# Performance work log

Hardware: AMD Instinct MI355X
Metric: run time of the kernel (lower is better)

The kernel has to match this reference:

```python
import jax, jax.numpy as jnp
from jax import lax
import numpy as np

T, B, H, L = 512, 64, 512, 2


def _ran_layer(x, c0, w_ih, w_hh, b, length):
    """x: [T,B,H], c0: [B,H]; returns (output [T,B,H], c_T [B,H])."""
    wi = jnp.einsum('tbi,ih->tbh', x, w_ih)  # precompute input projections

    def step(c, inp):
        t, x_t, wi_t = inp
        g = c @ w_hh + b + wi_t                      # [B, 2H]
        f, i = jnp.split(g, 2, axis=1)
        c1 = jax.nn.sigmoid(i) * x_t + jax.nn.sigmoid(f) * jnp.tanh(c)
        mask = (t < length)[:, None].astype(c1.dtype)  # length-mask blend
        c1 = c1 * mask + c * (1.0 - mask)
        return c1, c1

    ts = jnp.arange(x.shape[0])
    cT, out = lax.scan(step, c0, (ts, x, wi))
    return out, cT


def setup_inputs() -> dict:
    key = jax.random.key(0)
    ks = jax.random.split(key, 8)
    stdv = 1.0 / np.sqrt(H)

    def u(k, shape):
        return jax.random.uniform(k, shape, jnp.float32, -stdv, stdv)

    return {
        'input_': jax.random.normal(ks[0], (T, B, H), jnp.float32),
        'hx': jnp.zeros((L, B, H), jnp.float32),
        'length': jax.random.randint(ks[1], (B,), 0, T, jnp.int64 if jax.config.jax_enable_x64 else jnp.int32),
        'w_ih_0': u(ks[2], (H, 2 * H)),
        'w_hh_0': u(ks[3], (H, 2 * H)),
        'b_0': jnp.zeros((2 * H,), jnp.float32),
        'w_ih_1': u(ks[4], (H, 2 * H)),
        'w_hh_1': u(ks[5], (H, 2 * H)),
        'b_1': jnp.zeros((2 * H,), jnp.float32),
    }


def reference(input_, hx, length, w_ih_0, w_hh_0, b_0, w_ih_1, w_hh_1, b_1):
    params = [(w_ih_0, w_hh_0, b_0), (w_ih_1, w_hh_1, b_1)]
    x = input_
    c_n = []
    for layer in range(L):
        w_ih, w_hh, b = params[layer]
        x, cT = _ran_layer(x, hx[layer], w_ih, w_hh, b, length)
        c_n.append(cT)
    return x, jnp.stack(c_n, 0)
```

## Files before the change

### kernel.cpp

```cpp
#include <hip/hip_runtime.h>

#define T_ 512
#define B_ 64
#define H_ 512
#define G_ 1024

typedef _Float16 f16;
typedef _Float16 h2 __attribute__((ext_vector_type(2)));
typedef _Float16 h4 __attribute__((ext_vector_type(4)));
typedef _Float16 f16x8 __attribute__((ext_vector_type(8)));
typedef float f32x4 __attribute__((ext_vector_type(4)));
typedef unsigned long long u64;

#define SPINMAX (1 << 22)

__device__ __forceinline__ float dot8_h(uint4 w, uint4 c, float acc) {
    union U { uint4 u; h2 h[4]; };
    U uw; uw.u = w;
    U uc; uc.u = c;
#if defined(__has_builtin) && __has_builtin(__builtin_amdgcn_fdot2)
    acc = __builtin_amdgcn_fdot2(uw.h[0], uc.h[0], acc, false);
    acc = __builtin_amdgcn_fdot2(uw.h[1], uc.h[1], acc, false);
    acc = __builtin_amdgcn_fdot2(uw.h[2], uc.h[2], acc, false);
    acc = __builtin_amdgcn_fdot2(uw.h[3], uc.h[3], acc, false);
#else
#pragma unroll
    for (int i = 0; i < 4; ++i) {
        acc += (float)uw.h[i][0] * (float)uc.h[i][0];
        acc += (float)uw.h[i][1] * (float)uc.h[i][1];
    }
#endif
    return acc;
}

__device__ __forceinline__ float sigm(float x) { return 1.f / (1.f + __expf(-x)); }

__device__ __forceinline__ u64 ldA64(const u64* p) {
    return __hip_atomic_load(p, __ATOMIC_RELAXED, __HIP_MEMORY_SCOPE_AGENT);
}
__device__ __forceinline__ void stA32(unsigned* p, unsigned v) {
    __hip_atomic_store(p, v, __ATOMIC_RELAXED, __HIP_MEMORY_SCOPE_AGENT);
}

__global__ void pack_fp16(const float* __restrict__ src, uint4* __restrict__ dst) {
    int idx = blockIdx.x * 256 + threadIdx.x;
    int j  = idx & (G_ - 1);
    int k8 = idx >> 10;
    union U { uint4 u; f16 h[8]; } v;
#pragma unroll
    for (int i = 0; i < 8; ++i)
        v.h[i] = (f16)src[(size_t)(k8 * 8 + i) * G_ + j];
    dst[idx] = v.u;
}

__global__ void pack_wcols(const float* __restrict__ src, uint4* __restrict__ dst) {
    int idx = blockIdx.x * 256 + threadIdx.x;
    int col = idx & 1023, k2 = idx >> 10;
    union U { uint4 u; f16 h[8]; } v;
#pragma unroll
    for (int i = 0; i < 8; ++i)
        v.h[i] = (f16)src[(size_t)(k2 * 8 + i) * G_ + col];
    dst[(size_t)col * 64 + k2] = v.u;
}

__global__ void pack_xf16(const float* __restrict__ src, f16* __restrict__ dst) {
    int idx = blockIdx.x * 256 + threadIdx.x;
    float4 a = ((const float4*)src)[idx * 2];
    float4 b = ((const float4*)src)[idx * 2 + 1];
    f16x8 v = {(f16)a.x, (f16)a.y, (f16)a.z, (f16)a.w,
               (f16)b.x, (f16)b.y, (f16)b.z, (f16)b.w};
    *(f16x8*)&dst[idx * 8] = v;
}

__global__ void pack_wT(const float* __restrict__ w, f16* __restrict__ bt) {
    int idx = blockIdx.x * 256 + threadIdx.x;
    int k = idx & 511, n = idx >> 9;
    bt[idx] = (f16)w[(size_t)k * G_ + n];
}

__launch_bounds__(256, 2)
__global__ void mfma_gemm(const f16* __restrict__ A, const f16* __restrict__ BT,
                          const float* __restrict__ bias, f16* __restrict__ C) {
    __shared__ __align__(16) f16 aLds[128][64 + 8];
    __shared__ __align__(16) f16 bLds[128][64 + 8];
    const int tid = threadIdx.x;
    const int bm = blockIdx.x, bn = blockIdx.y;
    const int lane = tid & 63, wid = tid >> 6;
    const int wm = wid & 1, wn = wid >> 1;
    const int fr = lane & 15, fg = lane >> 4;

    f32x4 acc[4][4] = {};

    for (int kt = 0; kt < 8; ++kt) {
#pragma unroll
        for (int p = 0; p < 4; ++p) {
            int i = p * 256 + tid;
            int row = i >> 3, slot = i & 7;
            uint4 av = *(const uint4*)&A[((size_t)(bm * 128 + row)) * 512 + kt * 64 + slot * 8];
            uint4 bv = *(const uint4*)&BT[((size_t)(bn * 128 + row)) * 512 + kt * 64 + slot * 8];
            *(uint4*)&aLds[row][slot * 8] = av;
            *(uint4*)&bLds[row][slot * 8] = bv;
        }
        __syncthreads();
#pragma unroll
        for (int kf = 0; kf < 2; ++kf) {
            const int k0 = kf * 32 + fg * 8;
            f16x8 af[4], bf[4];
#pragma unroll
            for (int mi = 0; mi < 4; ++mi)
                af[mi] = *(const f16x8*)&aLds[wm * 64 + mi * 16 + fr][k0];
#pragma unroll
            for (int ni = 0; ni < 4; ++ni)
                bf[ni] = *(const f16x8*)&bLds[wn * 64 + ni * 16 + fr][k0];
#pragma unroll
            for (int mi = 0; mi < 4; ++mi)
#pragma unroll
                for (int ni = 0; ni < 4; ++ni)
                    acc[mi][ni] = __builtin_amdgcn_mfma_f32_16x16x32_f16(
                        af[mi], bf[ni], acc[mi][ni], 0, 0, 0);
        }
        __syncthreads();
    }

#pragma unroll
    for (int mi = 0; mi < 4; ++mi) {
#pragma unroll
        for (int ni = 0; ni < 4; ++ni) {
            int n = bn * 128 + wn * 64 + ni * 16 + fr;
            float bv = bias[n];
#pragma unroll
            for (int r = 0; r < 4; ++r) {
                int m = bm * 128 + wm * 64 + mi * 16 + fg * 4 + r;
                C[(size_t)m * G_ + n] = (f16)(acc[mi][ni][r] + bv);
            }
        }
    }
}

#define GM 128
#define GN 64
#define GK 16
__launch_bounds__(256)
__global__ void gemm_bias_f16(const float* __restrict__ A,
                              const float* __restrict__ Bm,
                              const float* __restrict__ bias,
                              f16* __restrict__ C, int M) {
    __shared__ __align__(16) float Als[GK][GM + 4];
    __shared__ __align__(16) float Bls[GK][GN];
    int tid = threadIdx.x;
    int m_base = blockIdx.x * GM;
    int n_base = blockIdx.y * GN;
    int tx = tid & 15, ty = tid >> 4;
    int m0 = ty * 8, n0 = tx * 4;
    float acc[8][4] = {};

    for (int k0 = 0; k0 < H_; k0 += GK) {
#pragma unroll
        for (int r = 0; r < 2; ++r) {
            int idx2 = tid + 256 * r;
            int row = idx2 >> 2, kc = (idx2 & 3) * 4;
            float4 av = *(const float4*)&A[(size_t)(m_base + row) * H_ + k0 + kc];
            Als[kc + 0][row] = av.x;
            Als[kc + 1][row] = av.y;
            Als[kc + 2][row] = av.z;
            Als[kc + 3][row] = av.w;
        }
        {
            int kk = tid >> 4, colb = (tid & 15) * 4;
            float4 bv = *(const float4*)&Bm[(size_t)(k0 + kk) * G_ + n_base + colb];
            *(float4*)&Bls[kk][colb] = bv;
        }
        __syncthreads();
#pragma unroll
        for (int kk = 0; kk < GK; ++kk) {
            float a0[8], b0[4];
            *(float4*)&a0[0] = *(const float4*)&Als[kk][m0];
            *(float4*)&a0[4] = *(const float4*)&Als[kk][m0 + 4];
            *(float4*)&b0[0] = *(const float4*)&Bls[kk][n0];
#pragma unroll
            for (int im = 0; im < 8; ++im)
#pragma unroll
                for (int in = 0; in < 4; ++in)
                    acc[im][in] += a0[im] * b0[in];
        }
        __syncthreads();
    }
    float bv[4];
    *(float4*)&bv[0] = *(const float4*)&bias[n_base + n0];
#pragma unroll
    for (int im = 0; im < 8; ++im) {
        h4 hv;
#pragma unroll
        for (int in = 0; in < 4; ++in) hv[in] = (f16)(acc[im][in] + bv[in]);
        *(h4*)&C[(size_t)(m_base + m0 + im) * G_ + n_base + n0] = hv;
    }
}

template <int PATH>
__launch_bounds__(1024, 1)
__global__ void ran_scan(const float* __restrict__ x_in, float* __restrict__ x_out,
                         float* __restrict__ c_out, const float* __restrict__ c0,
                         const int* __restrict__ length,
                         const uint4* __restrict__ whh_p,
                         const f16* __restrict__ wi, const float* __restrict__ bias,
                         const float* __restrict__ whh_f, const float* __restrict__ wih_f) {
    __shared__ __align__(16) f16 c_h[H_];
    __shared__ __align__(16) float c_f32[H_];
    __shared__ __align__(16) float x_f32[H_];
    __shared__ float g_i_lds[H_];

    const int b = blockIdx.x, tid = threadIdx.x;
    int len = length[b];
    if (len < 0) len = 0;
    if (len > T_) len = T_;

    float c1 = 0.f;
    if (tid < H_) {
        c1 = c0[(size_t)b * H_ + tid];
        c_h[tid] = (f16)c1;
        if (PATH == 2) c_f32[tid] = c1;
    }
    const float bj = (PATH == 0) ? 0.f : bias[tid];
    __syncthreads();

    for (int t = 0; t < len; ++t) {
        const size_t base = ((size_t)t * B_ + b) * H_;
        float xv = 0.f;
        if (tid < H_) {
            xv = x_in[base + tid];
            if (PATH == 2) x_f32[tid] = xv;
        }
        if (PATH == 2) __syncthreads();

        float g;
        if (PATH == 0) g = (float)wi[((size_t)t * B_ + b) * G_ + tid];
        else           g = bj;

        if (PATH == 0) {
            const uint4* cc = (const uint4*)c_h;
#pragma unroll 4
            for (int k8 = 0; k8 < H_ / 8; ++k8)
                g = dot8_h(whh_p[(size_t)k8 * G_ + tid], cc[k8], g);
        } else {
#pragma unroll 2
            for (int k = 0; k < H_; k += 4) {
                float4 cv = *(const float4*)&c_f32[k];
                g += cv.x * whh_f[(size_t)(k + 0) * G_ + tid];
                g += cv.y * whh_f[(size_t)(k + 1) * G_ + tid];
                g += cv.z * whh_f[(size_t)(k + 2) * G_ + tid];
                g += cv.w * whh_f[(size_t)(k + 3) * G_ + tid];
            }
#pragma unroll 2
            for (int k = 0; k < H_; k += 4) {
                float4 xvv = *(const float4*)&x_f32[k];
                g += xvv.x * wih_f[(size_t)(k + 0) * G_ + tid];
                g += xvv.y * wih_f[(size_t)(k + 1) * G_ + tid];
                g += xvv.z * wih_f[(size_t)(k + 2) * G_ + tid];
                g += xvv.w * wih_f[(size_t)(k + 3) * G_ + tid];
            }
        }

        if (tid >= H_) g_i_lds[tid - H_] = g;
        __syncthreads();
        if (tid < H_) {
            float gi = g_i_lds[tid];
            float c_old = c1;
            c1 = sigm(gi) * xv + sigm(g) * tanhf(c_old);
            c_h[tid] = (f16)c1;
            if (PATH == 2) c_f32[tid] = c1;
            x_out[base + tid] = c1;
        }
        __syncthreads();
    }

    if (tid < H_) {
        for (int t = len; t < T_; ++t)
            x_out[((size_t)t * B_ + b) * H_ + tid] = c1;
        c_out[(size_t)b * H_ + tid] = c1;
    }
}

__global__ __launch_bounds__(512, 1)
void scan_mfma(const float* __restrict__ x_in, const f16* __restrict__ wi,
               const uint4* __restrict__ wpack, const float* __restrict__ c0,
               const int* __restrict__ length, float* __restrict__ out,
               float* __restrict__ cn, unsigned* __restrict__ cbuf,
               int base_tag) {
    __shared__ __align__(16) f16 c_h[2][H_];
    __shared__ __align__(16) float2 g_buf[128];
    __shared__ float c_fin[2][64];

    const int tid = threadIdx.x;
    const int bg = blockIdx.x & 31, s = blockIdx.x >> 5;
    const int b0 = bg * 2;
    const int w = tid >> 6, lane = tid & 63;
    const int n16 = lane & 15, kg = lane >> 4;

    const int gc = w * 16 + n16;
    const int gcol = (gc < 64) ? (s * 64 + gc) : (512 + s * 64 + (gc - 64));
    uint4 wreg[16];
    {
        const uint4* wp = wpack + (size_t)gcol * 64 + kg;
#pragma unroll
        for (int m = 0; m < 16; ++m) wreg[m] = wp[m * 4];
    }

    {
        float a = c0[(size_t)b0 * H_ + tid];
        float b = c0[(size_t)(b0 + 1) * H_ + tid];
        c_h[0][tid] = (f16)a;
        c_h[1][tid] = (f16)b;
    }
    int len0 = length[b0], len1 = length[b0 + 1];
    len0 = min(max(len0, 0), T_);
    len1 = min(max(len1, 0), T_);
    const int maxlen = max(len0, len1);

    const int ab = (n16 < 2) ? n16 : 1;
    const int fb = tid >> 6, fcol = tid & 63;
    const int jj = s * 64 + fcol;
    const int myb = b0 + fb;
    const int mylen = fb ? len1 : len0;
    float c_old = 0.f;
    if (tid < 128) c_old = c0[(size_t)myb * H_ + jj];
    __syncthreads();

    for (int t = 0; t < maxlen; ++t) {
        float xv = 0.f, wif = 0.f, wii = 0.f;
        if (tid < 128) {
            size_t rb = (size_t)t * B_ + myb;
            xv  = x_in[rb * H_ + jj];
            wif = (float)wi[rb * G_ + jj];
            wii = (float)wi[rb * G_ + 512 + jj];
        }

        {
            f32x4 acc = {};
#pragma unroll
            for (int m = 0; m < 16; ++m) {
                f16x8 af = *(const f16x8*)&c_h[ab][m * 32 + kg * 8];
                acc = __builtin_amdgcn_mfma_f32_16x16x32_f16(
                    af, *(const f16x8*)&wreg[m], acc, 0, 0, 0);
            }
            if (lane < 16)
                g_buf[w * 16 + lane] = make_float2(acc[0], acc[1]);
        }
        __syncthreads();

        const int p1 = (t + 1) & 1;
        const unsigned tagw = (unsigned)(base_tag + t + 1) & 0xffffu;

        if (tid < 128) {
            float2 vf = g_buf[fcol];
            float2 vi = g_buf[64 + fcol];
            float gf = (fb ? vf.y : vf.x) + wif;
            float gi = (fb ? vi.y : vi.x) + wii;
            float c1;
            if (t < mylen) {
                float e2 = __expf(2.f * c_old);
                float th = (e2 - 1.f) / (e2 + 1.f);
                c1 = sigm(gi) * xv + sigm(gf) * th;
            } else {
                c1 = c_old;
            }
            c_old = c1;
            union { f16 h; unsigned short u; } cv;
            cv.h = (f16)c1;
            stA32(&cbuf[((size_t)(p1 * B_ + myb) << 9) + jj],
                  (tagw << 16) | (unsigned)cv.u);
            out[((size_t)t * B_ + myb) * H_ + jj] = c1;
            c_h[fb][jj] = cv.h;
        }

        if (t + 1 < maxlen) {
            int bidx = tid >> 8;
            int e = (tid & 255) * 2;
            if ((unsigned)(e - s * 64) >= 64u) {
                const u64 want2 = ((u64)tagw << 48) | ((u64)tagw << 16);
                const u64 mask2 = 0xffff0000ffff0000ull;
                const u64* pb = (const u64*)(cbuf +
                                   ((size_t)(p1 * B_ + b0 + bidx) << 9) + e);
                u64 v = ldA64(pb);
                int gd = 0;
                while ((v & mask2) != want2) {
                    if (++gd > SPINMAX) break;
                    if (gd > 16) __builtin_amdgcn_s_sleep(2);
                    v = ldA64(pb);
                }
                unsigned lo = (unsigned)v & 0xffffu;
                unsigned hi = (unsigned)(v >> 32) & 0xffffu;
                *(unsigned*)&c_h[bidx][e] = lo | (hi << 16);
            }
        }
        __syncthreads();
    }

    if (tid < 128) {
        c_fin[fb][fcol] = c_old;
        cn[(size_t)myb * H_ + jj] = c_old;
    }
    __syncthreads();

    const int ntail = T_ - maxlen;
    for (int i = tid; i < ntail * 128; i += 512) {
        int tb = i >> 7;
        int cc = i & 127;
        int tfb = cc >> 6, tfc = cc & 63;
        out[((size_t)(maxlen + tb) * B_ + b0 + tfb) * H_ + s * 64 + tfc] =
            c_fin[tfb][tfc];
    }
}

__global__ __launch_bounds__(512, 1)
void scan_vgpr(const float* __restrict__ x_in, const f16* __restrict__ wi,
               const uint4* __restrict__ wpack, const float* __restrict__ c0,
               const int* __restrict__ length, float* __restrict__ out,
               float* __restrict__ cn, unsigned* __restrict__ cbuf,
               int base_tag) {
    __shared__ __align__(16) f16 c_h[2][H_];
    __shared__ float red[2][128][5];
    __shared__ float c_fin[2][64];

    const int tid = threadIdx.x;
    const int bg = blockIdx.x & 31, s = blockIdx.x >> 5;
    const int b0 = bg * 2;
    const int col = tid & 127, kq = tid >> 7;

    const int gcol = s * 64 + (col & 63) + ((col >> 6) << 9);
    uint4 wreg[16];
    {
        const uint4* wp = wpack + (size_t)gcol * 64 + kq * 16;
#pragma unroll
        for (int i = 0; i < 16; ++i) wreg[i] = wp[i];
    }

    {
        float a = c0[(size_t)b0 * H_ + tid];
        float b = c0[(size_t)(b0 + 1) * H_ + tid];
        c_h[0][tid] = (f16)a;
        c_h[1][tid] = (f16)b;
    }
    int len0 = length[b0], len1 = length[b0 + 1];
    len0 = min(max(len0, 0), T_);
    len1 = min(max(len1, 0), T_);
    const int maxlen = max(len0, len1);

    const int fb = tid >> 6, fcol = tid & 63;
    const int jj = s * 64 + fcol;
    const int myb = b0 + fb;
    const int mylen = fb ? len1 : len0;
    float c_old = 0.f;
    if (tid < 128) c_old = c0[(size_t)myb * H_ + jj];
    __syncthreads();

    for (int t = 0; t < maxlen; ++t) {
        float xv = 0.f, wif = 0.f, wii = 0.f;
        if (tid < 128) {
            size_t rb = (size_t)t * B_ + myb;
            xv  = x_in[rb * H_ + jj];
            wif = (float)wi[rb * G_ + jj];
            wii = (float)wi[rb * G_ + 512 + jj];
        }

        {
            const uint4* cA = (const uint4*)&c_h[0][0];
            const uint4* cB = (const uint4*)&c_h[1][0];
            const int k20 = kq * 16;
            float a0 = 0.f, a1 = 0.f;
#pragma unroll
            for (int k = 0; k < 16; ++k) {
                uint4 cav = cA[k20 + k];
                uint4 cbv = cB[k20 + k];
                a0 = dot8_h(wreg[k], cav, a0);
                a1 = dot8_h(wreg[k], cbv, a1);
            }
            red[0][col][kq] = a0;
            red[1][col][kq] = a1;
        }
        __syncthreads();

        const int p1 = (t + 1) & 1;
        const unsigned tagw = (unsigned)(base_tag + t + 1) & 0xffffu;

        if (tid < 128) {
            float gf = red[fb][fcol][0] + red[fb][fcol][1] +
                       red[fb][fcol][2] + red[fb][fcol][3] + wif;
            float gi = red[fb][64 + fcol][0] + red[fb][64 + fcol][1] +
                       red[fb][64 + fcol][2] + red[fb][64 + fcol][3] + wii;
            float c1;
            if (t < mylen) {
                float e2 = __expf(2.f * c_old);
                float th = (e2 - 1.f) / (e2 + 1.f);
                c1 = sigm(gi) * xv + sigm(gf) * th;
            } else {
                c1 = c_old;
            }
            c_old = c1;
            union { f16 h; unsigned short u; } cv;
            cv.h = (f16)c1;
            stA32(&cbuf[((size_t)(p1 * B_ + myb) << 9) + jj],
                  (tagw << 16) | (unsigned)cv.u);
            out[((size_t)t * B_ + myb) * H_ + jj] = c1;
            c_h[fb][jj] = cv.h;
        }

        if (t + 1 < maxlen) {
            int bidx = tid >> 8;
            int e = (tid & 255) * 2;
            if ((unsigned)(e - s * 64) >= 64u) {
                const u64 want2 = ((u64)tagw << 48) | ((u64)tagw << 16);
                const u64 mask2 = 0xffff0000ffff0000ull;
                const u64* pb = (const u64*)(cbuf +
                                   ((size_t)(p1 * B_ + b0 + bidx) << 9) + e);
                u64 v = ldA64(pb);
                int gd = 0;
                while ((v & mask2) != want2) {
                    if (++gd > SPINMAX) break;
                    if (gd > 16) __builtin_amdgcn_s_sleep(2);
                    v = ldA64(pb);
                }
                unsigned lo = (unsigned)v & 0xffffu;
                unsigned hi = (unsigned)(v >> 32) & 0xffffu;
                *(unsigned*)&c_h[bidx][e] = lo | (hi << 16);
            }
        }
        __syncthreads();
    }

    if (tid < 128) {
        c_fin[fb][fcol] = c_old;
        cn[(size_t)myb * H_ + jj] = c_old;
    }
    __syncthreads();

    const int ntail = T_ - maxlen;
    for (int i = tid; i < ntail * 128; i += 512) {
        int tb = i >> 7;
        int cc = i & 127;
        int tfb = cc >> 6, tfc = cc & 63;
        out[((size_t)(maxlen + tb) * B_ + b0 + tfb) * H_ + s * 64 + tfc] =
            c_fin[tfb][tfc];
    }
}

extern "C" void kernel_launch(void* const* d_in, const int* in_sizes, int n_in,
                              void* d_out, int out_size, void* d_ws, size_t ws_size,
                              hipStream_t stream) {
    const float* input_ = (const float*)d_in[0];
    const float* hx     = (const float*)d_in[1];
    const int*   length = (const int*)d_in[2];
    const float* w_ih_0 = (const float*)d_in[3];
    const float* w_hh_0 = (const float*)d_in[4];
    const float* b_0    = (const float*)d_in[5];
    const float* w_ih_1 = (const float*)d_in[6];
    const float* w_hh_1 = (const float*)d_in[7];
    const float* b_1    = (const float*)d_in[8];

    float* out = (float*)d_out;
    float* cn  = out + (size_t)T_ * B_ * H_;

    char* wsb = (char*)d_ws;
    const size_t MB = 1u << 20;
    const size_t WI_BYTES = (size_t)T_ * B_ * G_ * sizeof(f16);
    const size_t XH_BYTES = (size_t)T_ * B_ * H_ * sizeof(f16);
    const int M = T_ * B_;

    const size_t need1 = WI_BYTES + XH_BYTES + 2 * MB + 256 * 1024;
    const size_t need2 = WI_BYTES + MB + 256 * 1024;
    const size_t needA = 2 * MB + WI_BYTES;

    if (ws_size >= need1) {
        f16*      wi    = (f16*)wsb;
        f16*      xh    = (f16*)(wsb + WI_BYTES);
        uint4*    wpack = (uint4*)(wsb + WI_BYTES + XH_BYTES);
        f16*      bt    = (f16*)(wsb + WI_BYTES + XH_BYTES + MB);
        unsigned* cbuf  = (unsigned*)(wsb + WI_BYTES + XH_BYTES + 2 * MB);

        hipMemsetAsync(cbuf, 0, 256 * 1024, stream);

        pack_wcols<<<256, 256, 0, stream>>>(w_hh_0, wpack);
        pack_xf16<<<8192, 256, 0, stream>>>(input_, xh);
        pack_wT<<<2048, 256, 0, stream>>>(w_ih_0, bt);
        mfma_gemm<<<dim3(M / 128, G_ / 128), 256, 0, stream>>>(xh, bt, b_0, wi);
        scan_mfma<<<256, 512, 0, stream>>>(input_, wi, wpack, hx, length,
                                           out, cn, cbuf, 0);
        pack_wcols<<<256, 256, 0, stream>>>(w_hh_1, wpack);
        pack_xf16<<<8192, 256, 0, stream>>>(out, xh);
        pack_wT<<<2048, 256, 0, stream>>>(w_ih_1, bt);
        mfma_gemm<<<dim3(M / 128, G_ / 128), 256, 0, stream>>>(xh, bt, b_1, wi);
        scan_mfma<<<256, 512, 0, stream>>>(out, wi, wpack,
                                           hx + (size_t)B_ * H_, length,
                                           out, cn + (size_t)B_ * H_, cbuf, T_);
    } else if (ws_size >= need2) {
        f16*      wi    = (f16*)wsb;
        uint4*    wpack = (uint4*)(wsb + WI_BYTES);
        unsigned* cbuf  = (unsigned*)(wsb + WI_BYTES + MB);

        hipMemsetAsync(cbuf, 0, 256 * 1024, stream);

        pack_wcols<<<256, 256, 0, stream>>>(w_hh_0, wpack);
        gemm_bias_f16<<<dim3(M / GM, G_ / GN), 256, 0, stream>>>(input_, w_ih_0, b_0, wi, M);
        scan_vgpr<<<256, 512, 0, stream>>>(input_, wi, wpack, hx, length,
                                           out, cn, cbuf, 0);
        pack_wcols<<<256, 256, 0, stream>>>(w_hh_1, wpack);
        gemm_bias_f16<<<dim3(M / GM, G_ / GN), 256, 0, stream>>>(out, w_ih_1, b_1, wi, M);
        scan_vgpr<<<256, 512, 0, stream>>>(out, wi, wpack,
                                           hx + (size_t)B_ * H_, length,
                                           out, cn + (size_t)B_ * H_, cbuf, T_);
    } else if (ws_size >= needA) {
        uint4* whh0 = (uint4*)(wsb + 0 * MB);
        uint4* whh1 = (uint4*)(wsb + 1 * MB);
        f16* wi = (f16*)(wsb + 2 * MB);
        pack_fp16<<<256, 256, 0, stream>>>(w_hh_0, whh0);
        pack_fp16<<<256, 256, 0, stream>>>(w_hh_1, whh1);

        gemm_bias_f16<<<dim3(M / GM, G_ / GN), 256, 0, stream>>>(input_, w_ih_0, b_0, wi, M);
        ran_scan<0><<<64, 1024, 0, stream>>>(input_, out, cn, hx, length,
                                             whh0, wi, b_0, nullptr, nullptr);
        gemm_bias_f16<<<dim3(M / GM, G_ / GN), 256, 0, stream>>>(out, w_ih_1, b_1, wi, M);
        ran_scan<0><<<64, 1024, 0, stream>>>(out, out, cn + (size_t)B_ * H_,
                                             hx + (size_t)B_ * H_, length,
                                             whh1, wi, b_1, nullptr, nullptr);
    } else {
        ran_scan<2><<<64, 1024, 0, stream>>>(input_, out, cn, hx, length,
                                             nullptr, nullptr, b_0, w_hh_0, w_ih_0);
        ran_scan<2><<<64, 1024, 0, stream>>>(out, out, cn + (size_t)B_ * H_,
                                             hx + (size_t)B_ * H_, length,
                                             nullptr, nullptr, b_1, w_hh_1, w_ih_1);
    }
}
```

Measured before the change: 1.603 ms.

## Reorganize MFMA scan so gate pairs meet in-wave, dropping one block barrier

Replaces scan_mfma with scan_mfma6. Each wave now computes both the forget and input gate columns for the same 8 hidden units, and the two gates are combined with a cross-lane shuffle instead of going through an LDS buffer and an extra __syncthreads. The recurrent state is double-buffered in LDS by timestep parity, with padding between the two batch rows. Eight lanes per wave then finish both batch rows, which means more serial work for fewer threads, and the spin-wait now starts sleeping after more polls.

```diff
diff --git a/kernel.cpp b/kernel.cpp
--- a/kernel.cpp
+++ b/kernel.cpp
@@ -281,28 +281,162 @@
 }
 
 __global__ __launch_bounds__(512, 1)
-void scan_mfma(const float* __restrict__ x_in, const f16* __restrict__ wi,
+void scan_mfma6(const float* __restrict__ x_in, const f16* __restrict__ wi,
+                const uint4* __restrict__ wpack, const float* __restrict__ c0,
+                const int* __restrict__ length, float* __restrict__ out,
+                float* __restrict__ cn, unsigned* __restrict__ cbuf,
+                int base_tag) {
+    __shared__ __align__(16) f16 c_h[2][2][H_ + 32];
+    __shared__ float c_fin[2][64];
+
+    const int tid = threadIdx.x;
+    const int bg = blockIdx.x & 31, s = blockIdx.x >> 5;
+    const int b0 = bg * 2;
+    const int w = tid >> 6, lane = tid & 63;
+    const int n16 = lane & 15, kg = lane >> 4;
+
+    const int jloc = w * 8 + (n16 & 7);
+    const int gcol = (n16 < 8) ? (s * 64 + jloc) : (512 + s * 64 + jloc);
+    uint4 wreg[16];
+    {
+        const uint4* wp = wpack + (size_t)gcol * 64 + kg;
+#pragma unroll
+        for (int m = 0; m < 16; ++m) wreg[m] = wp[m * 4];
+    }
+
+    {
+        float a = c0[(size_t)b0 * H_ + tid];
+        float b = c0[(size_t)(b0 + 1) * H_ + tid];
+        c_h[0][0][tid] = (f16)a;
+        c_h[0][1][tid + 32] = (f16)b;
+    }
+    int len0 = length[b0], len1 = length[b0 + 1];
+    len0 = min(max(len0, 0), T_);
+    len1 = min(max(len1, 0), T_);
+    const int maxlen = max(len0, len1);
+
+    const int ab = (n16 < 1) ? 0 : 1;
+    const bool fin = (lane < 8);
+    const int jj = s * 64 + jloc;
+    float c_old0 = 0.f, c_old1 = 0.f;
+    if (fin) {
+        c_old0 = c0[(size_t)b0 * H_ + jj];
+        c_old1 = c0[(size_t)(b0 + 1) * H_ + jj];
+    }
+    __syncthreads();
+
+    for (int t = 0; t < maxlen; ++t) {
+        const int p = t & 1, p1 = p ^ 1;
+        float xv0 = 0.f, xv1 = 0.f, wif0 = 0.f, wif1 = 0.f, wii0 = 0.f, wii1 = 0.f;
+        if (fin) {
+            size_t r0 = (size_t)t * B_ + b0;
+            xv0  = x_in[r0 * H_ + jj];
+            xv1  = x_in[(r0 + 1) * H_ + jj];
+            wif0 = (float)wi[r0 * G_ + jj];
+            wif1 = (float)wi[(r0 + 1) * G_ + jj];
+            wii0 = (float)wi[r0 * G_ + 512 + jj];
+            wii1 = (float)wi[(r0 + 1) * G_ + 512 + jj];
+        }
+
+        f32x4 acc = {};
+        {
+            const f16* cb = &c_h[p][ab][ab ? 32 : 0];
+#pragma unroll
+            for (int m = 0; m < 16; ++m) {
+                f16x8 af = *(const f16x8*)(cb + m * 32 + kg * 8);
+                acc = __builtin_amdgcn_mfma_f32_16x16x32_f16(
+                    af, *(const f16x8*)&wreg[m], acc, 0, 0, 0);
+            }
+        }
+        const unsigned tagw = (unsigned)(base_tag + t + 1) & 0xffffu;
+
+        float gi0 = __shfl(acc[0], lane + 8, 64);
+        float gi1 = __shfl(acc[1], lane + 8, 64);
+
+        if (fin) {
+            float gf0 = acc[0] + wif0, gf1 = acc[1] + wif1;
+            gi0 += wii0; gi1 += wii1;
+            float c1_0, c1_1;
+            if (t < len0) {
+                float e2 = __expf(2.f * c_old0);
+                c1_0 = sigm(gi0) * xv0 + sigm(gf0) * ((e2 - 1.f) / (e2 + 1.f));
+            } else c1_0 = c_old0;
+            if (t < len1) {
+                float e2 = __expf(2.f * c_old1);
+                c1_1 = sigm(gi1) * xv1 + sigm(gf1) * ((e2 - 1.f) / (e2 + 1.f));
+            } else c1_1 = c_old1;
+            c_old0 = c1_0; c_old1 = c1_1;
+            union { f16 h; unsigned short u; } v0, v1;
+            v0.h = (f16)c1_0; v1.h = (f16)c1_1;
+            stA32(&cbuf[((size_t)(p1 * B_ + b0) << 9) + jj], (tagw << 16) | v0.u);
+            stA32(&cbuf[((size_t)(p1 * B_ + b0 + 1) << 9) + jj], (tagw << 16) | v1.u);
+            size_t ob = (size_t)t * B_ + b0;
+            out[ob * H_ + jj]       = c1_0;
+            out[(ob + 1) * H_ + jj] = c1_1;
+            c_h[p1][0][jj]      = v0.h;
+            c_h[p1][1][jj + 32] = v1.h;
+        }
+
+        if (t + 1 < maxlen) {
+            int bidx = tid >> 8;
+            int e = (tid & 255) * 2;
+            if ((unsigned)(e - s * 64) >= 64u) {
+                const u64 want2 = ((u64)tagw << 48) | ((u64)tagw << 16);
+                const u64 mask2 = 0xffff0000ffff0000ull;
+                const u64* pb = (const u64*)(cbuf +
+                                   ((size_t)(p1 * B_ + b0 + bidx) << 9) + e);
+                u64 v = ldA64(pb);
+                int gd = 0;
+                while ((v & mask2) != want2) {
+                    if (++gd > SPINMAX) break;
+                    if (gd > 128) __builtin_amdgcn_s_sleep(1);
+                    v = ldA64(pb);
+                }
+                *(unsigned*)&c_h[p1][bidx][e + (bidx ? 32 : 0)] =
+                    ((unsigned)v & 0xffffu) | (((unsigned)(v >> 32) & 0xffffu) << 16);
+            }
+        }
+        __syncthreads();
+    }
+
+    if (fin) {
+        c_fin[0][jloc] = c_old0;
+        c_fin[1][jloc] = c_old1;
+        cn[(size_t)b0 * H_ + jj]       = c_old0;
+        cn[(size_t)(b0 + 1) * H_ + jj] = c_old1;
+    }
+    __syncthreads();
+
+    const int ntail = T_ - maxlen;
+    for (int i = tid; i < ntail * 128; i += 512) {
+        int tb = i >> 7, cc = i & 127;
+        int q = cc >> 6, jl = cc & 63;
+        out[((size_t)(maxlen + tb) * B_ + b0 + q) * H_ + s * 64 + jl] =
+            c_fin[q][jl];
+    }
+}
+
+__global__ __launch_bounds__(512, 1)
+void scan_vgpr(const float* __restrict__ x_in, const f16* __restrict__ wi,
                const uint4* __restrict__ wpack, const float* __restrict__ c0,
                const int* __restrict__ length, float* __restrict__ out,
                float* __restrict__ cn, unsigned* __restrict__ cbuf,
                int base_tag) {
     __shared__ __align__(16) f16 c_h[2][H_];
-    __shared__ __align__(16) float2 g_buf[128];
+    __shared__ float red[2][128][5];
     __shared__ float c_fin[2][64];
 
     const int tid = threadIdx.x;
     const int bg = blockIdx.x & 31, s = blockIdx.x >> 5;
     const int b0 = bg * 2;
-    const int w = tid >> 6, lane = tid & 63;
-    const int n16 = lane & 15, kg = lane >> 4;
-
-    const int gc = w * 16 + n16;
-    const int gcol = (gc < 64) ? (s * 64 + gc) : (512 + s * 64 + (gc - 64));
+    const int col = tid & 127, kq = tid >> 7;
+
+    const int gcol = s * 64 + (col & 63) + ((col >> 6) << 9);
     uint4 wreg[16];
     {
-        const uint4* wp = wpack + (size_t)gcol * 64 + kg;
-#pragma unroll
-        for (int m = 0; m < 16; ++m) wreg[m] = wp[m * 4];
+        const uint4* wp = wpack + (size_t)gcol * 64 + kq * 16;
+#pragma unroll
+        for (int i = 0; i < 16; ++i) wreg[i] = wp[i];
     }
 
     {
@@ -316,7 +450,6 @@
     len1 = min(max(len1, 0), T_);
     const int maxlen = max(len0, len1);
 
-    const int ab = (n16 < 2) ? n16 : 1;
     const int fb = tid >> 6, fcol = tid & 63;
     const int jj = s * 64 + fcol;
     const int myb = b0 + fb;
@@ -335,15 +468,19 @@
         }
 
         {
-            f32x4 acc = {};
-#pragma unroll
-            for (int m = 0; m < 16; ++m) {
-                f16x8 af = *(const f16x8*)&c_h[ab][m * 32 + kg * 8];
-                acc = __builtin_amdgcn_mfma_f32_16x16x32_f16(
-                    af, *(const f16x8*)&wreg[m], acc, 0, 0, 0);
-            }
-            if (lane < 16)
-                g_buf[w * 16 + lane] = make_float2(acc[0], acc[1]);
+            const uint4* cA = (const uint4*)&c_h[0][0];
+            const uint4* cB = (const uint4*)&c_h[1][0];
+            const int k20 = kq * 16;
+            float a0 = 0.f, a1 = 0.f;
+#pragma unroll
+            for (int k = 0; k < 16; ++k) {
+                uint4 cav = cA[k20 + k];
+                uint4 cbv = cB[k20 + k];
+                a0 = dot8_h(wreg[k], cav, a0);
+                a1 = dot8_h(wreg[k], cbv, a1);
+            }
+            red[0][col][kq] = a0;
+            red[1][col][kq] = a1;
         }
         __syncthreads();
 
@@ -351,10 +488,10 @@
         const unsigned tagw = (unsigned)(base_tag + t + 1) & 0xffffu;
 
         if (tid < 128) {
-            float2 vf = g_buf[fcol];
-            float2 vi = g_buf[64 + fcol];
-            float gf = (fb ? vf.y : vf.x) + wif;
-            float gi = (fb ? vi.y : vi.x) + wii;
+            float gf = red[fb][fcol][0] + red[fb][fcol][1] +
+                       red[fb][fcol][2] + red[fb][fcol][3] + wif;
+            float gi = red[fb][64 + fcol][0] + red[fb][64 + fcol][1] +
+                       red[fb][64 + fcol][2] + red[fb][64 + fcol][3] + wii;
             float c1;
             if (t < mylen) {
                 float e2 = __expf(2.f * c_old);
@@ -411,138 +548,6 @@
     }
 }
 
-__global__ __launch_bounds__(512, 1)
-void scan_vgpr(const float* __restrict__ x_in, const f16* __restrict__ wi,
-               const uint4* __restrict__ wpack, const float* __restrict__ c0,
-               const int* __restrict__ length, float* __restrict__ out,
-               float* __restrict__ cn, unsigned* __restrict__ cbuf,
-               int base_tag) {
-    __shared__ __align__(16) f16 c_h[2][H_];
-    __shared__ float red[2][128][5];
-    __shared__ float c_fin[2][64];
-
-    const int tid = threadIdx.x;
-    const int bg = blockIdx.x & 31, s = blockIdx.x >> 5;
-    const int b0 = bg * 2;
-    const int col = tid & 127, kq = tid >> 7;
-
-    const int gcol = s * 64 + (col & 63) + ((col >> 6) << 9);
-    uint4 wreg[16];
-    {
-        const uint4* wp = wpack + (size_t)gcol * 64 + kq * 16;
-#pragma unroll
-        for (int i = 0; i < 16; ++i) wreg[i] = wp[i];
-    }
-
-    {
-        float a = c0[(size_t)b0 * H_ + tid];
-        float b = c0[(size_t)(b0 + 1) * H_ + tid];
-        c_h[0][tid] = (f16)a;
-        c_h[1][tid] = (f16)b;
-    }
-    int len0 = length[b0], len1 = length[b0 + 1];
-    len0 = min(max(len0, 0), T_);
-    len1 = min(max(len1, 0), T_);
-    const int maxlen = max(len0, len1);
-
-    const int fb = tid >> 6, fcol = tid & 63;
-    const int jj = s * 64 + fcol;
-    const int myb = b0 + fb;
-    const int mylen = fb ? len1 : len0;
-    float c_old = 0.f;
-    if (tid < 128) c_old = c0[(size_t)myb * H_ + jj];
-    __syncthreads();
-
-    for (int t = 0; t < maxlen; ++t) {
-        float xv = 0.f, wif = 0.f, wii = 0.f;
-        if (tid < 128) {
-            size_t rb = (size_t)t * B_ + myb;
-            xv  = x_in[rb * H_ + jj];
-            wif = (float)wi[rb * G_ + jj];
-            wii = (float)wi[rb * G_ + 512 + jj];
-        }
-
-        {
-            const uint4* cA = (const uint4*)&c_h[0][0];
-            const uint4* cB = (const uint4*)&c_h[1][0];
-            const int k20 = kq * 16;
-            float a0 = 0.f, a1 = 0.f;
-#pragma unroll
-            for (int k = 0; k < 16; ++k) {
-                uint4 cav = cA[k20 + k];
-                uint4 cbv = cB[k20 + k];
-                a0 = dot8_h(wreg[k], cav, a0);
-                a1 = dot8_h(wreg[k], cbv, a1);
-            }
-            red[0][col][kq] = a0;
-            red[1][col][kq] = a1;
-        }
-        __syncthreads();
-
-        const int p1 = (t + 1) & 1;
-        const unsigned tagw = (unsigned)(base_tag + t + 1) & 0xffffu;
-
-        if (tid < 128) {
-            float gf = red[fb][fcol][0] + red[fb][fcol][1] +
-                       red[fb][fcol][2] + red[fb][fcol][3] + wif;
-            float gi = red[fb][64 + fcol][0] + red[fb][64 + fcol][1] +
-                       red[fb][64 + fcol][2] + red[fb][64 + fcol][3] + wii;
-            float c1;
-            if (t < mylen) {
-                float e2 = __expf(2.f * c_old);
-                float th = (e2 - 1.f) / (e2 + 1.f);
-                c1 = sigm(gi) * xv + sigm(gf) * th;
-            } else {
-                c1 = c_old;
-            }
-            c_old = c1;
-            union { f16 h; unsigned short u; } cv;
-            cv.h = (f16)c1;
-            stA32(&cbuf[((size_t)(p1 * B_ + myb) << 9) + jj],
-                  (tagw << 16) | (unsigned)cv.u);
-            out[((size_t)t * B_ + myb) * H_ + jj] = c1;
-            c_h[fb][jj] = cv.h;
-        }
-
-        if (t + 1 < maxlen) {
-            int bidx = tid >> 8;
-            int e = (tid & 255) * 2;
-            if ((unsigned)(e - s * 64) >= 64u) {
-                const u64 want2 = ((u64)tagw << 48) | ((u64)tagw << 16);
-                const u64 mask2 = 0xffff0000ffff0000ull;
-                const u64* pb = (const u64*)(cbuf +
-                                   ((size_t)(p1 * B_ + b0 + bidx) << 9) + e);
-                u64 v = ldA64(pb);
-                int gd = 0;
-                while ((v & mask2) != want2) {
-                    if (++gd > SPINMAX) break;
-                    if (gd > 16) __builtin_amdgcn_s_sleep(2);
-                    v = ldA64(pb);
-                }
-                unsigned lo = (unsigned)v & 0xffffu;
-                unsigned hi = (unsigned)(v >> 32) & 0xffffu;
-                *(unsigned*)&c_h[bidx][e] = lo | (hi << 16);
-            }
-        }
-        __syncthreads();
-    }
-
-    if (tid < 128) {
-        c_fin[fb][fcol] = c_old;
-        cn[(size_t)myb * H_ + jj] = c_old;
-    }
-    __syncthreads();
-
-    const int ntail = T_ - maxlen;
-    for (int i = tid; i < ntail * 128; i += 512) {
-        int tb = i >> 7;
-        int cc = i & 127;
-        int tfb = cc >> 6, tfc = cc & 63;
-        out[((size_t)(maxlen + tb) * B_ + b0 + tfb) * H_ + s * 64 + tfc] =
-            c_fin[tfb][tfc];
-    }
-}
-
 extern "C" void kernel_launch(void* const* d_in, const int* in_sizes, int n_in,
                               void* d_out, int out_size, void* d_ws, size_t ws_size,
                               hipStream_t stream) {
@@ -582,15 +587,15 @@
         pack_xf16<<<8192, 256, 0, stream>>>(input_, xh);
         pack_wT<<<2048, 256, 0, stream>>>(w_ih_0, bt);
         mfma_gemm<<<dim3(M / 128, G_ / 128), 256, 0, stream>>>(xh, bt, b_0, wi);
-        scan_mfma<<<256, 512, 0, stream>>>(input_, wi, wpack, hx, length,
-                                           out, cn, cbuf, 0);
+        scan_mfma6<<<256, 512, 0, stream>>>(input_, wi, wpack, hx, length,
+                                            out, cn, cbuf, 0);
         pack_wcols<<<256, 256, 0, stream>>>(w_hh_1, wpack);
         pack_xf16<<<8192, 256, 0, stream>>>(out, xh);
         pack_wT<<<2048, 256, 0, stream>>>(w_ih_1, bt);
         mfma_gemm<<<dim3(M / 128, G_ / 128), 256, 0, stream>>>(xh, bt, b_1, wi);
-        scan_mfma<<<256, 512, 0, stream>>>(out, wi, wpack,
-                                           hx + (size_t)B_ * H_, length,
-                                           out, cn + (size_t)B_ * H_, cbuf, T_);
+        scan_mfma6<<<256, 512, 0, stream>>>(out, wi, wpack,
+                                            hx + (size_t)B_ * H_, length,
+                                            out, cn + (size_t)B_ * H_, cbuf, T_);
     } else if (ws_size >= need2) {
         f16*      wi    = (f16*)wsb;
         uint4*    wpack = (uint4*)(wsb + WI_BYTES);
```

Result: slower. 2.682 ms (+67.3%).
